# Kernel tuning notes

Hardware: AMD Instinct MI355X
Metric: run time of the kernel (lower is better)

## Reference

```python
import jax, jax.numpy as jnp
import numpy as np

N, E, H, R = 16384, 262144, 256, 64
INV_SQRT_3 = 1.0 / np.sqrt(3.0)
INV_SQRT_H = 1.0 / np.sqrt(float(H))
INV_SQRT_2 = 1.0 / np.sqrt(2.0)


def ssilu(t):
    # ScaledSiLU: silu(x) / 0.6
    return jax.nn.silu(t) * (1.0 / 0.6)


def layernorm(x, g, b):
    m = jnp.mean(x, axis=-1, keepdims=True)
    v = jnp.var(x, axis=-1, keepdims=True)
    return (x - m) * jax.lax.rsqrt(v + 1e-5) * g + b


def gated_equivariant_block(x, v, Wv1, Wv2, Wu1, bu1, Wu2, bu2, out_ch):
    # x: [N, Cin], v: [N, 3, Cin]
    vec1 = jnp.linalg.norm(v @ Wv1, axis=-2)          # [N, Cin]
    vec2 = v @ Wv2                                     # [N, 3, out_ch]
    h = ssilu(jnp.concatenate([x, vec1], axis=-1) @ Wu1 + bu1) @ Wu2 + bu2
    xn, vn = h[..., :out_ch], h[..., out_ch:]
    return ssilu(xn), vn[:, None, :] * vec2


def setup_inputs() -> dict:
    key = jax.random.key(0)
    ks = iter(jax.random.split(key, 48))

    def w(shape, fan_in):
        return jax.random.normal(next(ks), shape, jnp.float32) / np.sqrt(float(fan_in))

    return {
        "x": jax.random.normal(next(ks), (N, H), jnp.float32),
        "vec": jax.random.normal(next(ks), (N, 3, H), jnp.float32),
        "edge_rbf": jax.random.uniform(next(ks), (E, R), jnp.float32),
        "edge_vector": jax.random.normal(next(ks), (E, 3), jnp.float32),
        # PaiNNMessage params
        "ln_g": jnp.ones((H,), jnp.float32), "ln_b": jnp.zeros((H,), jnp.float32),
        "W_x1": w((H, H), H), "b_x1": jnp.zeros((H,), jnp.float32),
        "W_x2": w((H, 3 * H), H), "b_x2": jnp.zeros((3 * H,), jnp.float32),
        "W_rbf": w((R, 3 * H), R), "b_rbf": jnp.zeros((3 * H,), jnp.float32),
        # PaiNNUpdate params
        "W_vp": w((H, 2 * H), H),
        "W_xv1": w((2 * H, H), 2 * H), "b_xv1": jnp.zeros((H,), jnp.float32),
        "W_xv2": w((H, 3 * H), H), "b_xv2": jnp.zeros((3 * H,), jnp.float32),
        # PaiNNOutput block 1 (H -> H//2)
        "o1_Wv1": w((H, H), H), "o1_Wv2": w((H, H // 2), H),
        "o1_Wu1": w((2 * H, H), 2 * H), "o1_bu1": jnp.zeros((H,), jnp.float32),
        "o1_Wu2": w((H, H), H), "o1_bu2": jnp.zeros((H,), jnp.float32),
        # PaiNNOutput block 2 (H//2 -> 1)
        "o2_Wv1": w((H // 2, H // 2), H // 2), "o2_Wv2": w((H // 2, 1), H // 2),
        "o2_Wu1": w((H, H // 2), H), "o2_bu1": jnp.zeros((H // 2,), jnp.float32),
        "o2_Wu2": w((H // 2, 2), H // 2), "o2_bu2": jnp.zeros((2,), jnp.float32),
        "edge_index": jax.random.randint(next(ks), (2, E), 0, N),
    }


def reference(x, vec, edge_rbf, edge_vector,
              ln_g, ln_b, W_x1, b_x1, W_x2, b_x2, W_rbf, b_rbf,
              W_vp, W_xv1, b_xv1, W_xv2, b_xv2,
              o1_Wv1, o1_Wv2, o1_Wu1, o1_bu1, o1_Wu2, o1_bu2,
              o2_Wv1, o2_Wv2, o2_Wu1, o2_bu1, o2_Wu2, o2_bu2,
              edge_index):
    src, dst = edge_index[0], edge_index[1]

    # ---- PaiNNMessage ----
    xh = ssilu(layernorm(x, ln_g, ln_b) @ W_x1 + b_x1) @ W_x2 + b_x2   # [N, 3H]
    rbfh = edge_rbf @ W_rbf + b_rbf                                     # [E, 3H]
    m = xh[src] * rbfh                                                  # gather + fuse
    m1, m2, m3 = m[:, :H], m[:, H:2 * H], m[:, 2 * H:]
    m2 = m2 * INV_SQRT_3
    vmsg = (vec[src] * m2[:, None, :] + m3[:, None, :] * edge_vector[:, :, None]) * INV_SQRT_H  # [E,3,H]
    dx = jax.ops.segment_sum(m1, dst, num_segments=N)
    dvec = jax.ops.segment_sum(vmsg, dst, num_segments=N)
    x = x + dx
    vec = vec + dvec

    # ---- PaiNNUpdate ----
    vp = vec @ W_vp                                    # [N, 3, 2H]
    vec1, vec2 = vp[..., :H], vp[..., H:]
    vec_dot = jnp.sum(vec1 * vec2, axis=1) * INV_SQRT_H            # [N, H]
    vnorm = jnp.sqrt(jnp.sum(vec2 * vec2, axis=-2) + 1e-8)          # [N, H]
    xvh = ssilu(jnp.concatenate([x, vnorm], axis=-1) @ W_xv1 + b_xv1) @ W_xv2 + b_xv2
    xv1, xv2, xv3 = xvh[:, :H], xvh[:, H:2 * H], xvh[:, 2 * H:]
    x = x + (xv1 + xv2 * vec_dot) * INV_SQRT_2
    vec = vec + xv3[:, None, :] * vec1

    # ---- PaiNNOutput ----
    x, vec = gated_equivariant_block(x, vec, o1_Wv1, o1_Wv2, o1_Wu1, o1_bu1, o1_Wu2, o1_bu2, H // 2)
    x, vec = gated_equivariant_block(x, vec, o2_Wv1, o2_Wv2, o2_Wu1, o2_bu1, o2_Wu2, o2_bu2, 1)
    return jnp.squeeze(vec, axis=-1)   # [N, 3]
```

## Files before the change

### kernel.cpp

```cpp
#include <hip/hip_runtime.h>
#include <math.h>

#define NN 16384
#define EE 262144
#define HH 256

#define INV_SQRT_3f 0.57735026918962576f
#define INV_SQRT_Hf 0.0625f
#define INV_SQRT_2f 0.70710678118654752f
#define SSILU_SCALE 1.6666666666666667f

typedef __attribute__((ext_vector_type(8))) short bf16x8;
typedef __attribute__((ext_vector_type(4))) float f32x4;

__device__ __forceinline__ float ssilu_f(float v) {
    return v * (1.0f / (1.0f + __expf(-v))) * SSILU_SCALE;
}
__device__ __forceinline__ float b2f(short s) {
    unsigned int u = ((unsigned int)(unsigned short)s) << 16;
    return __uint_as_float(u);
}
__device__ __forceinline__ short f2b(float f) {
    unsigned int u = __float_as_uint(f);
    unsigned int r = (u + 0x7fff + ((u >> 16) & 1)) >> 16;
    return (short)r;
}

__global__ void __launch_bounds__(256) ln_kernel(const float* __restrict__ x,
                                                 const float* __restrict__ g,
                                                 const float* __restrict__ b,
                                                 short* __restrict__ oh,
                                                 short* __restrict__ ol,
                                                 float* __restrict__ x1) {
    int n = blockIdx.x;
    int t = threadIdx.x;
    float v = x[(long)n * HH + t];
    x1[(long)n * HH + t] = v;
    float s = v, s2 = v * v;
    #pragma unroll
    for (int off = 32; off > 0; off >>= 1) {
        s  += __shfl_down(s, off);
        s2 += __shfl_down(s2, off);
    }
    __shared__ float red[8];
    int wave = t >> 6, lane = t & 63;
    if (lane == 0) { red[wave] = s; red[4 + wave] = s2; }
    __syncthreads();
    __shared__ float mr[2];
    if (t == 0) {
        float ts = red[0] + red[1] + red[2] + red[3];
        float ts2 = red[4] + red[5] + red[6] + red[7];
        float mean = ts * (1.0f / HH);
        float var = ts2 * (1.0f / HH) - mean * mean;
        mr[0] = mean;
        mr[1] = rsqrtf(var + 1e-5f);
    }
    __syncthreads();
    float o = (v - mr[0]) * mr[1] * g[t] + b[t];
    short hh = f2b(o);
    oh[(long)n * HH + t] = hh;
    ol[(long)n * HH + t] = f2b(o - b2f(hh));
}

struct WtArgs {
    const float* W[12];
    int K[12];
    int N[12];
    int off[13];
};

__global__ void __launch_bounds__(256) wt_split_all(WtArgs a,
                                                    short* __restrict__ WTh,
                                                    short* __restrict__ WTl) {
    int idx = blockIdx.x * 256 + threadIdx.x;
    int s = 0;
    #pragma unroll
    for (int i = 1; i < 12; i++) s += (idx >= a.off[i]) ? 1 : 0;
    int local = idx - a.off[s];
    int K = a.K[s], N = a.N[s];
    int k = local / N, n = local - k * N;
    float w = a.W[s][local];
    short hh = f2b(w);
    long o = (long)a.off[s] + (long)n * K + k;
    WTh[o] = hh;
    WTl[o] = f2b(w - b2f(hh));
}

__global__ void __launch_bounds__(256) split4_kernel(const float* __restrict__ in,
                                                     short* __restrict__ h,
                                                     short* __restrict__ l) {
    long i = ((long)blockIdx.x * 256 + threadIdx.x) * 4;
    float4 v = *(const float4*)(in + i);
    short4 oh, ol;
    oh.x = f2b(v.x); ol.x = f2b(v.x - b2f(oh.x));
    oh.y = f2b(v.y); ol.y = f2b(v.y - b2f(oh.y));
    oh.z = f2b(v.z); ol.z = f2b(v.z - b2f(oh.z));
    oh.w = f2b(v.w); ol.w = f2b(v.w - b2f(oh.w));
    *(short4*)(h + i) = oh;
    *(short4*)(l + i) = ol;
}

__global__ void __launch_bounds__(256) mfma_gemm(const short* __restrict__ Ah,
                                                 const short* __restrict__ Al,
                                                 const short* __restrict__ Wh,
                                                 const short* __restrict__ Wl,
                                                 const float* __restrict__ bias,
                                                 void* __restrict__ Ch,
                                                 short* __restrict__ Cl,
                                                 int M, int K, int N, int act) {
    int tid = threadIdx.x;
    int wave = tid >> 6, lane = tid & 63;
    int quad = lane >> 4, l16 = lane & 15;
    long bm = (long)blockIdx.x * 128 + wave * 32;
    long bn = (long)blockIdx.y * 64;
    long a0 = (bm + l16) * K + quad * 8;
    long a1 = a0 + (long)16 * K;
    long w0 = (bn + l16) * K + quad * 8;

    f32x4 acc[2][4];
    #pragma unroll
    for (int f = 0; f < 2; f++)
        #pragma unroll
        for (int t = 0; t < 4; t++) acc[f][t] = (f32x4){0.f, 0.f, 0.f, 0.f};

    bf16x8 cah[2], cal[2], cbh[4], cbl[4];
    cah[0] = *(const bf16x8*)(Ah + a0);
    cah[1] = *(const bf16x8*)(Ah + a1);
    cal[0] = *(const bf16x8*)(Al + a0);
    cal[1] = *(const bf16x8*)(Al + a1);
    #pragma unroll
    for (int t = 0; t < 4; t++) {
        long wo = w0 + (long)t * 16 * K;
        cbh[t] = *(const bf16x8*)(Wh + wo);
        cbl[t] = *(const bf16x8*)(Wl + wo);
    }

    for (int k0 = 0; k0 < K; k0 += 32) {
        int k1 = k0 + 32;
        bf16x8 nah[2], nal[2], nbh[4], nbl[4];
        if (k1 < K) {
            nah[0] = *(const bf16x8*)(Ah + a0 + k1);
            nah[1] = *(const bf16x8*)(Ah + a1 + k1);
            nal[0] = *(const bf16x8*)(Al + a0 + k1);
            nal[1] = *(const bf16x8*)(Al + a1 + k1);
            #pragma unroll
            for (int t = 0; t < 4; t++) {
                long wo = w0 + (long)t * 16 * K + k1;
                nbh[t] = *(const bf16x8*)(Wh + wo);
                nbl[t] = *(const bf16x8*)(Wl + wo);
            }
        }
        #pragma unroll
        for (int t = 0; t < 4; t++) {
            #pragma unroll
            for (int f = 0; f < 2; f++) {
                acc[f][t] = __builtin_amdgcn_mfma_f32_16x16x32_bf16(cah[f], cbh[t], acc[f][t], 0, 0, 0);
                acc[f][t] = __builtin_amdgcn_mfma_f32_16x16x32_bf16(cal[f], cbh[t], acc[f][t], 0, 0, 0);
                acc[f][t] = __builtin_amdgcn_mfma_f32_16x16x32_bf16(cah[f], cbl[t], acc[f][t], 0, 0, 0);
            }
        }
        if (k1 < K) {
            cah[0] = nah[0]; cah[1] = nah[1];
            cal[0] = nal[0]; cal[1] = nal[1];
            #pragma unroll
            for (int t = 0; t < 4; t++) { cbh[t] = nbh[t]; cbl[t] = nbl[t]; }
        }
    }

    #pragma unroll
    for (int f = 0; f < 2; f++) {
        long row0 = bm + f * 16 + quad * 4;
        #pragma unroll
        for (int t = 0; t < 4; t++) {
            long col = bn + t * 16 + l16;
            float bv = bias ? bias[col] : 0.f;
            #pragma unroll
            for (int r = 0; r < 4; r++) {
                float v = acc[f][t][r] + bv;
                if (act & 1) v = ssilu_f(v);
                long idx = (row0 + r) * N + col;
                if (Cl) {
                    short hh = f2b(v);
                    ((short*)Ch)[idx] = hh;
                    Cl[idx] = f2b(v - b2f(hh));
                } else if (act & 2) {
                    ((short*)Ch)[idx] = f2b(v);
                } else {
                    ((float*)Ch)[idx] = v;
                }
            }
        }
    }
}

__global__ void __launch_bounds__(256) zero_kernel(int* __restrict__ p, int n) {
    int i = blockIdx.x * 256 + threadIdx.x;
    if (i < n) p[i] = 0;
}

__global__ void __launch_bounds__(256) hist_kernel(const int* __restrict__ eidx,
                                                   int* __restrict__ cnt) {
    int e = blockIdx.x * 256 + threadIdx.x;
    atomicAdd(&cnt[eidx[EE + e]], 1);
}

__global__ void __launch_bounds__(256) scan_kernel(int* __restrict__ cursor,
                                                   int* __restrict__ rowptr) {
    int t = threadIdx.x;
    int base_i = t * 64;
    int tsum = 0;
    for (int i = 0; i < 64; i++) tsum += cursor[base_i + i];
    __shared__ int ls[256];
    ls[t] = tsum;
    __syncthreads();
    for (int off = 1; off < 256; off <<= 1) {
        int v = (t >= off) ? ls[t - off] : 0;
        __syncthreads();
        ls[t] += v;
        __syncthreads();
    }
    int running = ls[t] - tsum;
    for (int i = 0; i < 64; i++) {
        int c = cursor[base_i + i];
        rowptr[base_i + i] = running;
        cursor[base_i + i] = running;
        running += c;
    }
    if (t == 255) rowptr[NN] = running;
}

__global__ void __launch_bounds__(256) scatter_kernel(const int* __restrict__ eidx,
                                                      const float* __restrict__ ev,
                                                      int* __restrict__ cursor,
                                                      int* __restrict__ perm,
                                                      int* __restrict__ dsts,
                                                      int* __restrict__ srcs,
                                                      float* __restrict__ evs) {
    int e = blockIdx.x * 256 + threadIdx.x;
    int s_ = eidx[e];
    int d_ = eidx[EE + e];
    int pos = atomicAdd(&cursor[d_], 1);
    perm[pos] = e;
    dsts[pos] = d_;
    srcs[pos] = s_;
    evs[pos * 3 + 0] = ev[e * 3 + 0];
    evs[pos * 3 + 1] = ev[e * 3 + 1];
    evs[pos * 3 + 2] = ev[e * 3 + 2];
}

__global__ void __launch_bounds__(512) edge_gather_kernel(
        const float* __restrict__ rbf,
        const short* __restrict__ Wrh,
        const short* __restrict__ Wrl,
        const float* __restrict__ b_rbf,
        const float* __restrict__ xh,
        const float* __restrict__ vec,
        const int* __restrict__ perm,
        const int* __restrict__ dsts,
        const int* __restrict__ srcs,
        const float* __restrict__ evs,
        float* __restrict__ x1,
        float* __restrict__ vecacc) {
    int tid = threadIdx.x;
    int wave = tid >> 6, lane = tid & 63;
    int quad = lane >> 4, l16 = lane & 15;
    int bm = blockIdx.x * 128;
    int base = wave * 16;

    __shared__ __align__(16) float mlds[128][66];
    __shared__ int dst_s[128], src_s[128];
    __shared__ float ev_s[128][3];

    if (lane < 16) {
        int i = base + lane;
        dst_s[i] = dsts[bm + i];
        src_s[i] = srcs[bm + i];
        ev_s[i][0] = evs[(long)(bm + i) * 3 + 0];
        ev_s[i][1] = evs[(long)(bm + i) * 3 + 1];
        ev_s[i][2] = evs[(long)(bm + i) * 3 + 2];
    }

    int e0 = perm[bm + base + l16];
    bf16x8 afh[2], afl[2];
    {
        long ebase = (long)e0 * 64 + quad * 8;
        #pragma unroll
        for (int ks = 0; ks < 2; ks++) {
            float4 ua = *(const float4*)(rbf + ebase + ks * 32);
            float4 ub = *(const float4*)(rbf + ebase + ks * 32 + 4);
            float vv[8] = {ua.x, ua.y, ua.z, ua.w, ub.x, ub.y, ub.z, ub.w};
            bf16x8 hh, ll;
            #pragma unroll
            for (int j = 0; j < 8; j++) {
                short hb = f2b(vv[j]);
                hh[j] = hb;
                ll[j] = f2b(vv[j] - b2f(hb));
            }
            afh[ks] = hh;
            afl[ks] = ll;
        }
    }

    for (int sec = 0; sec < 3; sec++) {
        for (int tile = 0; tile < 4; tile++) {
            int bn = sec * 256 + tile * 64;
            f32x4 acc[4];
            #pragma unroll
            for (int t = 0; t < 4; t++) {
                float bv = b_rbf[bn + t * 16 + l16];
                acc[t] = (f32x4){bv, bv, bv, bv};
                #pragma unroll
                for (int ks = 0; ks < 2; ks++) {
                    long wo = (long)(bn + t * 16 + l16) * 64 + ks * 32 + quad * 8;
                    bf16x8 bh = *(const bf16x8*)(Wrh + wo);
                    bf16x8 bl = *(const bf16x8*)(Wrl + wo);
                    acc[t] = __builtin_amdgcn_mfma_f32_16x16x32_bf16(afh[ks], bh, acc[t], 0, 0, 0);
                    acc[t] = __builtin_amdgcn_mfma_f32_16x16x32_bf16(afl[ks], bh, acc[t], 0, 0, 0);
                    acc[t] = __builtin_amdgcn_mfma_f32_16x16x32_bf16(afh[ks], bl, acc[t], 0, 0, 0);
                }
            }
            #pragma unroll
            for (int t = 0; t < 4; t++)
                #pragma unroll
                for (int r = 0; r < 4; r++)
                    mlds[base + quad * 4 + r][t * 16 + l16] = acc[t][r];

            int colx = tile * 64 + lane;
            if (sec == 0) {
                float pv[16];
                #pragma unroll
                for (int i = 0; i < 16; i++) {
                    long xb = (long)src_s[base + i] * 768;
                    pv[i] = mlds[base + i][lane] * xh[xb + colx];
                }
                float a = 0.f;
                int dprev = dst_s[base];
                #pragma unroll
                for (int i = 0; i < 16; i++) {
                    int d = dst_s[base + i];
                    if (d != dprev) {
                        atomicAdd(&x1[(long)dprev * 256 + colx], a);
                        a = 0.f;
                        dprev = d;
                    }
                    a += pv[i];
                }
                atomicAdd(&x1[(long)dprev * 256 + colx], a);
            } else if (sec == 1) {
                float a0 = 0.f, a1 = 0.f, a2 = 0.f;
                int dprev = dst_s[base];
                #pragma unroll 1
                for (int b = 0; b < 4; b++) {
                    float p0[4], p1[4], p2[4];
                    #pragma unroll
                    for (int j = 0; j < 4; j++) {
                        int i = b * 4 + j;
                        long xb = (long)src_s[base + i] * 768;
                        float m2 = mlds[base + i][lane] * (INV_SQRT_3f * INV_SQRT_Hf) *
                                   xh[xb + 256 + colx];
                        p0[j] = vec[xb + colx] * m2;
                        p1[j] = vec[xb + 256 + colx] * m2;
                        p2[j] = vec[xb + 512 + colx] * m2;
                    }
                    #pragma unroll
                    for (int j = 0; j < 4; j++) {
                        int i = b * 4 + j;
                        int d = dst_s[base + i];
                        if (d != dprev) {
                            long vb = (long)dprev * 768 + colx;
                            atomicAdd(&vecacc[vb], a0);
                            atomicAdd(&vecacc[vb + 256], a1);
                            atomicAdd(&vecacc[vb + 512], a2);
                            a0 = a1 = a2 = 0.f;
                            dprev = d;
                        }
                        a0 += p0[j]; a1 += p1[j]; a2 += p2[j];
                    }
                }
                long vb = (long)dprev * 768 + colx;
                atomicAdd(&vecacc[vb], a0);
                atomicAdd(&vecacc[vb + 256], a1);
                atomicAdd(&vecacc[vb + 512], a2);
            } else {
                float pm[16];
                #pragma unroll
                for (int i = 0; i < 16; i++) {
                    long xb = (long)src_s[base + i] * 768;
                    pm[i] = mlds[base + i][lane] * INV_SQRT_Hf * xh[xb + 512 + colx];
                }
                float a0 = 0.f, a1 = 0.f, a2 = 0.f;
                int dprev = dst_s[base];
                #pragma unroll
                for (int i = 0; i < 16; i++) {
                    int d = dst_s[base + i];
                    if (d != dprev) {
                        long vb = (long)dprev * 768 + colx;
                        atomicAdd(&vecacc[vb], a0);
                        atomicAdd(&vecacc[vb + 256], a1);
                        atomicAdd(&vecacc[vb + 512], a2);
                        a0 = a1 = a2 = 0.f;
                        dprev = d;
                    }
                    a0 += pm[i] * ev_s[base + i][0];
                    a1 += pm[i] * ev_s[base + i][1];
                    a2 += pm[i] * ev_s[base + i][2];
                }
                long vb = (long)dprev * 768 + colx;
                atomicAdd(&vecacc[vb], a0);
                atomicAdd(&vecacc[vb + 256], a1);
                atomicAdd(&vecacc[vb + 512], a2);
            }
        }
    }
}

__global__ void __launch_bounds__(256) vdot_cat_kernel(const float* __restrict__ vec1,
                                                       const short* __restrict__ vec2,
                                                       const float* __restrict__ x1,
                                                       float* __restrict__ vdot,
                                                       short* __restrict__ cath,
                                                       short* __restrict__ catl) {
    int idx = blockIdx.x * 256 + threadIdx.x;
    int n = idx >> 8, h = idx & 255;
    float dsum = 0.f, s2 = 0.f;
    #pragma unroll
    for (int d = 0; d < 3; d++) {
        long r = (long)(n * 3 + d) * 256 + h;
        float a = vec1[r];
        float b = b2f(vec2[r]);
        dsum += a * b;
        s2 += b * b;
    }
    vdot[idx] = dsum * INV_SQRT_Hf;
    float xv = x1[idx];
    short hh = f2b(xv);
    cath[(long)n * 512 + h] = hh;
    catl[(long)n * 512 + h] = f2b(xv - b2f(hh));
    float vn = sqrtf(s2 + 1e-8f);
    short vh = f2b(vn);
    cath[(long)n * 512 + 256 + h] = vh;
    catl[(long)n * 512 + 256 + h] = f2b(vn - b2f(vh));
}

__global__ void __launch_bounds__(256) e4_kernel(float* __restrict__ x1,
                                                 float* __restrict__ vecacc,
                                                 const float* __restrict__ vec1,
                                                 const float* __restrict__ vdot,
                                                 const short* __restrict__ xvh_h,
                                                 const short* __restrict__ xvh_l) {
    int idx = blockIdx.x * 256 + threadIdx.x;
    int n = idx >> 8, h = idx & 255;
    long b0 = (long)n * 768 + h;
    float xv1 = b2f(xvh_h[b0])       + b2f(xvh_l[b0]);
    float xv2 = b2f(xvh_h[b0 + 256]) + b2f(xvh_l[b0 + 256]);
    float xv3 = b2f(xvh_h[b0 + 512]) + b2f(xvh_l[b0 + 512]);
    x1[idx] = x1[idx] + (xv1 + xv2 * vdot[idx]) * INV_SQRT_2f;
    #pragma unroll
    for (int d = 0; d < 3; d++) {
        long r = (long)(n * 3 + d) * 256 + h;
        vecacc[r] = vecacc[r] + xv3 * vec1[r];
    }
}

__global__ void __launch_bounds__(256) normcat_kernel(const float* __restrict__ xin,
                                                      const short* __restrict__ w,
                                                      short* __restrict__ cath,
                                                      short* __restrict__ catl,
                                                      int Cx, int C, int shift) {
    int idx = blockIdx.x * 256 + threadIdx.x;
    int cols = 1 << shift;
    int n = idx >> shift, c = idx & (cols - 1);
    float v;
    if (c < Cx) {
        v = xin[(long)n * Cx + c];
    } else {
        int cc = c - Cx;
        float s = 0.f;
        #pragma unroll
        for (int d = 0; d < 3; d++) {
            float a = b2f(w[(long)(n * 3 + d) * C + cc]);
            s += a * a;
        }
        v = sqrtf(s);
    }
    short hh = f2b(v);
    cath[idx] = hh;
    catl[idx] = f2b(v - b2f(hh));
}

__global__ void __launch_bounds__(256) gate1_kernel(const float* __restrict__ h1,
                                                    const short* __restrict__ w2h,
                                                    const short* __restrict__ w2l,
                                                    float* __restrict__ x3,
                                                    short* __restrict__ vecCh,
                                                    short* __restrict__ vecCl) {
    int idx = blockIdx.x * 256 + threadIdx.x;
    int n = idx >> 7, c = idx & 127;
    x3[idx] = ssilu_f(h1[(long)n * 256 + c]);
    float vn = h1[(long)n * 256 + 128 + c];
    #pragma unroll
    for (int d = 0; d < 3; d++) {
        long r = (long)(n * 3 + d) * 128 + c;
        float wv = b2f(w2h[r]) + b2f(w2l[r]);
        float v = vn * wv;
        short hh = f2b(v);
        vecCh[r] = hh;
        vecCl[r] = f2b(v - b2f(hh));
    }
}

__global__ void __launch_bounds__(256) g12_kernel(const short* __restrict__ vecCh,
                                                  const short* __restrict__ vecCl,
                                                  const float* __restrict__ Wv2,
                                                  float* __restrict__ w4) {
    int row = blockIdx.x * 4 + (threadIdx.x >> 6);
    int lane = threadIdx.x & 63;
    long r0 = (long)row * 128 + lane;
    float v0 = b2f(vecCh[r0]) + b2f(vecCl[r0]);
    float v1 = b2f(vecCh[r0 + 64]) + b2f(vecCl[r0 + 64]);
    float s = v0 * Wv2[lane] + v1 * Wv2[64 + lane];
    #pragma unroll
    for (int off = 32; off > 0; off >>= 1) s += __shfl_down(s, off);
    if (lane == 0) w4[row] = s;
}

__global__ void __launch_bounds__(256) final_kernel(const float* __restrict__ t5,
                                                    const float* __restrict__ Wu2,
                                                    const float* __restrict__ bu2,
                                                    const float* __restrict__ w4,
                                                    float* __restrict__ out) {
    int n = blockIdx.x * 4 + (threadIdx.x >> 6);
    int lane = threadIdx.x & 63;
    float s = t5[(long)n * 128 + lane] * Wu2[lane * 2 + 1] +
              t5[(long)n * 128 + 64 + lane] * Wu2[(64 + lane) * 2 + 1];
    #pragma unroll
    for (int off = 32; off > 0; off >>= 1) s += __shfl_down(s, off);
    float val = __shfl(s, 0) + bu2[1];
    if (lane < 3) out[(long)n * 3 + lane] = val * w4[(long)n * 3 + lane];
}

extern "C" void kernel_launch(void* const* d_in, const int* in_sizes, int n_in,
                              void* d_out, int out_size, void* d_ws, size_t ws_size,
                              hipStream_t stream) {
    const float* x          = (const float*)d_in[0];
    const float* vec        = (const float*)d_in[1];
    const float* edge_rbf   = (const float*)d_in[2];
    const float* edge_vector= (const float*)d_in[3];
    const float* ln_g       = (const float*)d_in[4];
    const float* ln_b       = (const float*)d_in[5];
    const float* W_x1       = (const float*)d_in[6];
    const float* b_x1       = (const float*)d_in[7];
    const float* W_x2       = (const float*)d_in[8];
    const float* b_x2       = (const float*)d_in[9];
    const float* W_rbf      = (const float*)d_in[10];
    const float* b_rbf      = (const float*)d_in[11];
    const float* W_vp       = (const float*)d_in[12];
    const float* W_xv1      = (const float*)d_in[13];
    const float* b_xv1      = (const float*)d_in[14];
    const float* W_xv2      = (const float*)d_in[15];
    const float* b_xv2      = (const float*)d_in[16];
    const float* o1_Wv1     = (const float*)d_in[17];
    const float* o1_Wv2     = (const float*)d_in[18];
    const float* o1_Wu1     = (const float*)d_in[19];
    const float* o1_bu1     = (const float*)d_in[20];
    const float* o1_Wu2     = (const float*)d_in[21];
    const float* o1_bu2     = (const float*)d_in[22];
    const float* o2_Wv1     = (const float*)d_in[23];
    const float* o2_Wv2     = (const float*)d_in[24];
    const float* o2_Wu1     = (const float*)d_in[25];
    const float* o2_bu1     = (const float*)d_in[26];
    const float* o2_Wu2     = (const float*)d_in[27];
    const float* o2_bu2     = (const float*)d_in[28];
    const int*   edge_index = (const int*)d_in[29];
    float* out = (float*)d_out;
    float* ws  = (float*)d_ws;

    const size_t S = (size_t)NN * 256;
    const size_t Q = S / 4;
    float* x1      = ws;
    float* vecacc  = ws + 4 * Q;
    short* wtb     = (short*)(ws + 16 * Q);
    const long WLO = 1114112;
    short* xln_h = (short*)(ws + 18 * Q);
    short* xln_l = (short*)(ws + 20 * Q);
    short* t1_h  = (short*)(ws + 22 * Q);
    short* t1_l  = (short*)(ws + 24 * Q);
    float* xh    = ws + 30 * Q;
    int* rowptr    = (int*)(ws + 48 * Q);
    int* cursor    = rowptr + (NN + 1);
    int* perm      = cursor + NN;
    int* dsts      = perm + EE;
    int* srcs      = dsts + EE;
    float* evs     = (float*)(srcs + EE);
    short* vah   = (short*)(ws + 18 * Q);
    short* val_  = (short*)(ws + 24 * Q);
    float* vec1  = ws + 30 * Q;
    short* vec2b = (short*)(ws + 42 * Q);
    float* vdot  = ws + 48 * Q;
    short* catb_h = (short*)(ws + 18 * Q);
    short* catb_l = (short*)(ws + 22 * Q);
    short* t2_h  = (short*)(ws + 26 * Q);
    short* t2_l  = (short*)(ws + 28 * Q);
    short* xvh_h = (short*)(ws + 18 * Q);
    short* xvh_l = (short*)(ws + 42 * Q);
    short* vah2  = (short*)(ws + 18 * Q);
    short* val2  = (short*)(ws + 24 * Q);
    short* w1b   = (short*)(ws + 30 * Q);
    short* w2_h  = (short*)(ws + 36 * Q);
    short* w2_l  = (short*)(ws + 39 * Q);
    short* cat2_h = (short*)(ws + 42 * Q);
    short* cat2_l = (short*)(ws + 46 * Q);
    short* t4_h  = (short*)(ws + 18 * Q);
    short* t4_l  = (short*)(ws + 20 * Q);
    float* h1    = ws + 22 * Q;
    float* x3    = ws + 26 * Q;
    short* vecC_h = (short*)(ws + 28 * Q);
    short* vecC_l = (short*)(ws + 31 * Q);
    short* w3b   = (short*)(ws + 34 * Q);
    float* w4    = ws + 37 * Q;
    short* cat3_h = (short*)(ws + 38 * Q);
    short* cat3_l = (short*)(ws + 40 * Q);
    float* t5    = ws + 42 * Q;

    short* WT_x1    = wtb;
    short* WT_x2    = wtb + 65536;
    short* WT_vp    = wtb + 262144;
    short* WT_xv1   = wtb + 393216;
    short* WT_xv2   = wtb + 524288;
    short* WT_o1Wv1 = wtb + 720896;
    short* WT_o1Wv2 = wtb + 786432;
    short* WT_o1Wu1 = wtb + 819200;
    short* WT_o1Wu2 = wtb + 950272;
    short* WT_o2Wv1 = wtb + 1015808;
    short* WT_o2Wu1 = wtb + 1032192;
    short* WT_rbf   = wtb + 1064960;

    WtArgs wa;
    const float* wsrc[12] = {W_x1, W_x2, W_vp, W_xv1, W_xv2, o1_Wv1, o1_Wv2,
                             o1_Wu1, o1_Wu2, o2_Wv1, o2_Wu1, W_rbf};
    int wk[12] = {256, 256, 256, 512, 256, 256, 256, 512, 256, 128, 256, 64};
    int wn[12] = {256, 768, 512, 256, 768, 256, 128, 256, 256, 128, 128, 768};
    int off = 0;
    for (int i = 0; i < 12; i++) {
        wa.W[i] = wsrc[i]; wa.K[i] = wk[i]; wa.N[i] = wn[i];
        wa.off[i] = off; off += wk[i] * wn[i];
    }
    wa.off[12] = off;
    wt_split_all<<<off / 256, 256, 0, stream>>>(wa, wtb, wtb + WLO);

    hipMemcpyAsync(vecacc, vec, 3 * S * sizeof(float), hipMemcpyDeviceToDevice, stream);

    ln_kernel<<<NN, 256, 0, stream>>>(x, ln_g, ln_b, xln_h, xln_l, x1);
    mfma_gemm<<<dim3(NN / 128, 4), 256, 0, stream>>>(xln_h, xln_l, WT_x1, WT_x1 + WLO,
                                                     b_x1, t1_h, t1_l, NN, 256, 256, 1);
    mfma_gemm<<<dim3(NN / 128, 12), 256, 0, stream>>>(t1_h, t1_l, WT_x2, WT_x2 + WLO,
                                                      b_x2, xh, nullptr, NN, 256, 768, 0);

    zero_kernel<<<(NN + 255) / 256, 256, 0, stream>>>(cursor, NN);
    hist_kernel<<<EE / 256, 256, 0, stream>>>(edge_index, cursor);
    scan_kernel<<<1, 256, 0, stream>>>(cursor, rowptr);
    scatter_kernel<<<EE / 256, 256, 0, stream>>>(edge_index, edge_vector, cursor,
                                                 perm, dsts, srcs, evs);
    edge_gather_kernel<<<EE / 128, 512, 0, stream>>>(
        edge_rbf, WT_rbf, WT_rbf + WLO, b_rbf, xh, vec,
        perm, dsts, srcs, evs, x1, vecacc);
    split4_kernel<<<3 * S / 1024, 256, 0, stream>>>(vecacc, vah, val_);

    mfma_gemm<<<dim3(3 * NN / 128, 4), 256, 0, stream>>>(vah, val_, WT_vp, WT_vp + WLO,
                                                         nullptr, vec1, nullptr,
                                                         3 * NN, 256, 256, 0);
    mfma_gemm<<<dim3(3 * NN / 128, 4), 256, 0, stream>>>(vah, val_, WT_vp + 65536,
                                                         WT_vp + WLO + 65536,
                                                         nullptr, vec2b, nullptr,
                                                         3 * NN, 256, 256, 2);
    vdot_cat_kernel<<<NN, 256, 0, stream>>>(vec1, vec2b, x1, vdot, catb_h, catb_l);
    mfma_gemm<<<dim3(NN / 128, 4), 256, 0, stream>>>(catb_h, catb_l, WT_xv1, WT_xv1 + WLO,
                                                     b_xv1, t2_h, t2_l, NN, 512, 256, 1);
    mfma_gemm<<<dim3(NN / 128, 12), 256, 0, stream>>>(t2_h, t2_l, WT_xv2, WT_xv2 + WLO,
                                                      b_xv2, xvh_h, xvh_l, NN, 256, 768, 0);
    e4_kernel<<<NN, 256, 0, stream>>>(x1, vecacc, vec1, vdot, xvh_h, xvh_l);

    split4_kernel<<<3 * S / 1024, 256, 0, stream>>>(vecacc, vah2, val2);
    mfma_gemm<<<dim3(3 * NN / 128, 4), 256, 0, stream>>>(vah2, val2, WT_o1Wv1, WT_o1Wv1 + WLO,
                                                         nullptr, w1b, nullptr,
                                                         3 * NN, 256, 256, 2);
    mfma_gemm<<<dim3(3 * NN / 128, 2), 256, 0, stream>>>(vah2, val2, WT_o1Wv2, WT_o1Wv2 + WLO,
                                                         nullptr, w2_h, w2_l,
                                                         3 * NN, 256, 128, 0);
    normcat_kernel<<<NN * 512 / 256, 256, 0, stream>>>(x1, w1b, cat2_h, cat2_l, 256, 256, 9);
    mfma_gemm<<<dim3(NN / 128, 4), 256, 0, stream>>>(cat2_h, cat2_l, WT_o1Wu1, WT_o1Wu1 + WLO,
                                                     o1_bu1, t4_h, t4_l, NN, 512, 256, 1);
    mfma_gemm<<<dim3(NN / 128, 4), 256, 0, stream>>>(t4_h, t4_l, WT_o1Wu2, WT_o1Wu2 + WLO,
                                                     o1_bu2, h1, nullptr, NN, 256, 256, 0);
    gate1_kernel<<<NN * 128 / 256, 256, 0, stream>>>(h1, w2_h, w2_l, x3, vecC_h, vecC_l);

    mfma_gemm<<<dim3(3 * NN / 128, 2), 256, 0, stream>>>(vecC_h, vecC_l, WT_o2Wv1,
                                                         WT_o2Wv1 + WLO, nullptr,
                                                         w3b, nullptr, 3 * NN, 128, 128, 2);
    g12_kernel<<<3 * NN / 4, 256, 0, stream>>>(vecC_h, vecC_l, o2_Wv2, w4);
    normcat_kernel<<<NN * 256 / 256, 256, 0, stream>>>(x3, w3b, cat3_h, cat3_l, 128, 128, 8);
    mfma_gemm<<<dim3(NN / 128, 2), 256, 0, stream>>>(cat3_h, cat3_l, WT_o2Wu1, WT_o2Wu1 + WLO,
                                                     o2_bu1, t5, nullptr, NN, 256, 128, 1);
    final_kernel<<<NN / 4, 256, 0, stream>>>(t5, o2_Wu2, o2_bu2, w4, out);
}
```

Before: 1.459 ms.

## Convert fp32 activations to bf16 hi/lo inside GEMM and merge sibling GEMMs

The GEMM now reads fp32 activations and splits them into bf16 hi/lo pairs in registers, so the split4 kernels and the hi/lo outputs of the producer kernels go away. The two W_vp GEMMs and the two o1 Wv GEMMs, which share the same input, are each merged into one launch with a wider N and a split epilogue. This cuts kernel launches and intermediate traffic. In exchange, the A loads double in bytes per element and the conversion ALU work is repeated in every N-tile block.

```diff
diff --git a/kernel.cpp b/kernel.cpp
--- a/kernel.cpp
+++ b/kernel.cpp
@@ -25,12 +25,20 @@
     unsigned int r = (u + 0x7fff + ((u >> 16) & 1)) >> 16;
     return (short)r;
 }
+__device__ __forceinline__ void cvt8(float4 a, float4 b, bf16x8& h, bf16x8& l) {
+    float v[8] = {a.x, a.y, a.z, a.w, b.x, b.y, b.z, b.w};
+    #pragma unroll
+    for (int j = 0; j < 8; j++) {
+        short hh = f2b(v[j]);
+        h[j] = hh;
+        l[j] = f2b(v[j] - b2f(hh));
+    }
+}
 
 __global__ void __launch_bounds__(256) ln_kernel(const float* __restrict__ x,
                                                  const float* __restrict__ g,
                                                  const float* __restrict__ b,
-                                                 short* __restrict__ oh,
-                                                 short* __restrict__ ol,
+                                                 float* __restrict__ o_,
                                                  float* __restrict__ x1) {
     int n = blockIdx.x;
     int t = threadIdx.x;
@@ -56,10 +64,7 @@
         mr[1] = rsqrtf(var + 1e-5f);
     }
     __syncthreads();
-    float o = (v - mr[0]) * mr[1] * g[t] + b[t];
-    short hh = f2b(o);
-    oh[(long)n * HH + t] = hh;
-    ol[(long)n * HH + t] = f2b(o - b2f(hh));
+    o_[(long)n * HH + t] = (v - mr[0]) * mr[1] * g[t] + b[t];
 }
 
 struct WtArgs {
@@ -86,27 +91,12 @@
     WTl[o] = f2b(w - b2f(hh));
 }
 
-__global__ void __launch_bounds__(256) split4_kernel(const float* __restrict__ in,
-                                                     short* __restrict__ h,
-                                                     short* __restrict__ l) {
-    long i = ((long)blockIdx.x * 256 + threadIdx.x) * 4;
-    float4 v = *(const float4*)(in + i);
-    short4 oh, ol;
-    oh.x = f2b(v.x); ol.x = f2b(v.x - b2f(oh.x));
-    oh.y = f2b(v.y); ol.y = f2b(v.y - b2f(oh.y));
-    oh.z = f2b(v.z); ol.z = f2b(v.z - b2f(oh.z));
-    oh.w = f2b(v.w); ol.w = f2b(v.w - b2f(oh.w));
-    *(short4*)(h + i) = oh;
-    *(short4*)(l + i) = ol;
-}
-
-__global__ void __launch_bounds__(256) mfma_gemm(const short* __restrict__ Ah,
-                                                 const short* __restrict__ Al,
+__global__ void __launch_bounds__(256) mfma_gemm(const float* __restrict__ A,
                                                  const short* __restrict__ Wh,
                                                  const short* __restrict__ Wl,
                                                  const float* __restrict__ bias,
-                                                 void* __restrict__ Ch,
-                                                 short* __restrict__ Cl,
+                                                 void* __restrict__ C1,
+                                                 void* __restrict__ C2,
                                                  int M, int K, int N, int act) {
     int tid = threadIdx.x;
     int wave = tid >> 6, lane = tid & 63;
@@ -124,10 +114,8 @@
         for (int t = 0; t < 4; t++) acc[f][t] = (f32x4){0.f, 0.f, 0.f, 0.f};
 
     bf16x8 cah[2], cal[2], cbh[4], cbl[4];
-    cah[0] = *(const bf16x8*)(Ah + a0);
-    cah[1] = *(const bf16x8*)(Ah + a1);
-    cal[0] = *(const bf16x8*)(Al + a0);
-    cal[1] = *(const bf16x8*)(Al + a1);
+    cvt8(*(const float4*)(A + a0), *(const float4*)(A + a0 + 4), cah[0], cal[0]);
+    cvt8(*(const float4*)(A + a1), *(const float4*)(A + a1 + 4), cah[1], cal[1]);
     #pragma unroll
     for (int t = 0; t < 4; t++) {
         long wo = w0 + (long)t * 16 * K;
@@ -137,12 +125,13 @@
 
     for (int k0 = 0; k0 < K; k0 += 32) {
         int k1 = k0 + 32;
-        bf16x8 nah[2], nal[2], nbh[4], nbl[4];
+        float4 n0a, n0b, n1a, n1b;
+        bf16x8 nbh[4], nbl[4];
         if (k1 < K) {
-            nah[0] = *(const bf16x8*)(Ah + a0 + k1);
-            nah[1] = *(const bf16x8*)(Ah + a1 + k1);
-            nal[0] = *(const bf16x8*)(Al + a0 + k1);
-            nal[1] = *(const bf16x8*)(Al + a1 + k1);
+            n0a = *(const float4*)(A + a0 + k1);
+            n0b = *(const float4*)(A + a0 + k1 + 4);
+            n1a = *(const float4*)(A + a1 + k1);
+            n1b = *(const float4*)(A + a1 + k1 + 4);
             #pragma unroll
             for (int t = 0; t < 4; t++) {
                 long wo = w0 + (long)t * 16 * K + k1;
@@ -160,8 +149,8 @@
             }
         }
         if (k1 < K) {
-            cah[0] = nah[0]; cah[1] = nah[1];
-            cal[0] = nal[0]; cal[1] = nal[1];
+            cvt8(n0a, n0b, cah[0], cal[0]);
+            cvt8(n1a, n1b, cah[1], cal[1]);
             #pragma unroll
             for (int t = 0; t < 4; t++) { cbh[t] = nbh[t]; cbl[t] = nbl[t]; }
         }
@@ -177,16 +166,25 @@
             #pragma unroll
             for (int r = 0; r < 4; r++) {
                 float v = acc[f][t][r] + bv;
-                if (act & 1) v = ssilu_f(v);
-                long idx = (row0 + r) * N + col;
-                if (Cl) {
-                    short hh = f2b(v);
-                    ((short*)Ch)[idx] = hh;
-                    Cl[idx] = f2b(v - b2f(hh));
-                } else if (act & 2) {
-                    ((short*)Ch)[idx] = f2b(v);
+                long row = row0 + r;
+                if (act == 4) {
+                    if (col < 256) ((float*)C1)[row * 256 + col] = v;
+                    else           ((short*)C2)[row * 256 + col - 256] = f2b(v);
+                } else if (act == 5) {
+                    if (col < 256) ((short*)C1)[row * 256 + col] = f2b(v);
+                    else           ((float*)C2)[row * 128 + col - 256] = v;
                 } else {
-                    ((float*)Ch)[idx] = v;
+                    long idx = row * N + col;
+                    if (act == 3) {
+                        short hh = f2b(v);
+                        ((short*)C1)[idx] = hh;
+                        ((short*)C2)[idx] = f2b(v - b2f(hh));
+                    } else if (act == 2) {
+                        ((short*)C1)[idx] = f2b(v);
+                    } else {
+                        if (act == 1) v = ssilu_f(v);
+                        ((float*)C1)[idx] = v;
+                    }
                 }
             }
         }
@@ -288,16 +286,7 @@
         for (int ks = 0; ks < 2; ks++) {
             float4 ua = *(const float4*)(rbf + ebase + ks * 32);
             float4 ub = *(const float4*)(rbf + ebase + ks * 32 + 4);
-            float vv[8] = {ua.x, ua.y, ua.z, ua.w, ub.x, ub.y, ub.z, ub.w};
-            bf16x8 hh, ll;
-            #pragma unroll
-            for (int j = 0; j < 8; j++) {
-                short hb = f2b(vv[j]);
-                hh[j] = hb;
-                ll[j] = f2b(vv[j] - b2f(hb));
-            }
-            afh[ks] = hh;
-            afl[ks] = ll;
+            cvt8(ua, ub, afh[ks], afl[ks]);
         }
     }
 
@@ -418,8 +407,7 @@
                                                        const short* __restrict__ vec2,
                                                        const float* __restrict__ x1,
                                                        float* __restrict__ vdot,
-                                                       short* __restrict__ cath,
-                                                       short* __restrict__ catl) {
+                                                       float* __restrict__ cat) {
     int idx = blockIdx.x * 256 + threadIdx.x;
     int n = idx >> 8, h = idx & 255;
     float dsum = 0.f, s2 = 0.f;
@@ -432,14 +420,8 @@
         s2 += b * b;
     }
     vdot[idx] = dsum * INV_SQRT_Hf;
-    float xv = x1[idx];
-    short hh = f2b(xv);
-    cath[(long)n * 512 + h] = hh;
-    catl[(long)n * 512 + h] = f2b(xv - b2f(hh));
-    float vn = sqrtf(s2 + 1e-8f);
-    short vh = f2b(vn);
-    cath[(long)n * 512 + 256 + h] = vh;
-    catl[(long)n * 512 + 256 + h] = f2b(vn - b2f(vh));
+    cat[(long)n * 512 + h] = x1[idx];
+    cat[(long)n * 512 + 256 + h] = sqrtf(s2 + 1e-8f);
 }
 
 __global__ void __launch_bounds__(256) e4_kernel(float* __restrict__ x1,
@@ -464,8 +446,7 @@
 
 __global__ void __launch_bounds__(256) normcat_kernel(const float* __restrict__ xin,
                                                       const short* __restrict__ w,
-                                                      short* __restrict__ cath,
-                                                      short* __restrict__ catl,
+                                                      float* __restrict__ cat,
                                                       int Cx, int C, int shift) {
     int idx = blockIdx.x * 256 + threadIdx.x;
     int cols = 1 << shift;
@@ -483,17 +464,13 @@
         }
         v = sqrtf(s);
     }
-    short hh = f2b(v);
-    cath[idx] = hh;
-    catl[idx] = f2b(v - b2f(hh));
+    cat[idx] = v;
 }
 
 __global__ void __launch_bounds__(256) gate1_kernel(const float* __restrict__ h1,
-                                                    const short* __restrict__ w2h,
-                                                    const short* __restrict__ w2l,
+                                                    const float* __restrict__ w2,
                                                     float* __restrict__ x3,
-                                                    short* __restrict__ vecCh,
-                                                    short* __restrict__ vecCl) {
+                                                    float* __restrict__ vecC) {
     int idx = blockIdx.x * 256 + threadIdx.x;
     int n = idx >> 7, c = idx & 127;
     x3[idx] = ssilu_f(h1[(long)n * 256 + c]);
@@ -501,24 +478,17 @@
     #pragma unroll
     for (int d = 0; d < 3; d++) {
         long r = (long)(n * 3 + d) * 128 + c;
-        float wv = b2f(w2h[r]) + b2f(w2l[r]);
-        float v = vn * wv;
-        short hh = f2b(v);
-        vecCh[r] = hh;
-        vecCl[r] = f2b(v - b2f(hh));
-    }
-}
-
-__global__ void __launch_bounds__(256) g12_kernel(const short* __restrict__ vecCh,
-                                                  const short* __restrict__ vecCl,
+        vecC[r] = vn * w2[r];
+    }
+}
+
+__global__ void __launch_bounds__(256) g12_kernel(const float* __restrict__ vecC,
                                                   const float* __restrict__ Wv2,
                                                   float* __restrict__ w4) {
     int row = blockIdx.x * 4 + (threadIdx.x >> 6);
     int lane = threadIdx.x & 63;
     long r0 = (long)row * 128 + lane;
-    float v0 = b2f(vecCh[r0]) + b2f(vecCl[r0]);
-    float v1 = b2f(vecCh[r0 + 64]) + b2f(vecCl[r0 + 64]);
-    float s = v0 * Wv2[lane] + v1 * Wv2[64 + lane];
+    float s = vecC[r0] * Wv2[lane] + vecC[r0 + 64] * Wv2[64 + lane];
     #pragma unroll
     for (int off = 32; off > 0; off >>= 1) s += __shfl_down(s, off);
     if (lane == 0) w4[row] = s;
@@ -581,10 +551,8 @@
     float* vecacc  = ws + 4 * Q;
     short* wtb     = (short*)(ws + 16 * Q);
     const long WLO = 1114112;
-    short* xln_h = (short*)(ws + 18 * Q);
-    short* xln_l = (short*)(ws + 20 * Q);
-    short* t1_h  = (short*)(ws + 22 * Q);
-    short* t1_l  = (short*)(ws + 24 * Q);
+    float* xln   = ws + 18 * Q;
+    float* t1    = ws + 22 * Q;
     float* xh    = ws + 30 * Q;
     int* rowptr    = (int*)(ws + 48 * Q);
     int* cursor    = rowptr + (NN + 1);
@@ -592,34 +560,23 @@
     int* dsts      = perm + EE;
     int* srcs      = dsts + EE;
     float* evs     = (float*)(srcs + EE);
-    short* vah   = (short*)(ws + 18 * Q);
-    short* val_  = (short*)(ws + 24 * Q);
     float* vec1  = ws + 30 * Q;
     short* vec2b = (short*)(ws + 42 * Q);
     float* vdot  = ws + 48 * Q;
-    short* catb_h = (short*)(ws + 18 * Q);
-    short* catb_l = (short*)(ws + 22 * Q);
-    short* t2_h  = (short*)(ws + 26 * Q);
-    short* t2_l  = (short*)(ws + 28 * Q);
+    float* cat   = ws + 18 * Q;
+    float* t2    = ws + 26 * Q;
     short* xvh_h = (short*)(ws + 18 * Q);
     short* xvh_l = (short*)(ws + 42 * Q);
-    short* vah2  = (short*)(ws + 18 * Q);
-    short* val2  = (short*)(ws + 24 * Q);
     short* w1b   = (short*)(ws + 30 * Q);
-    short* w2_h  = (short*)(ws + 36 * Q);
-    short* w2_l  = (short*)(ws + 39 * Q);
-    short* cat2_h = (short*)(ws + 42 * Q);
-    short* cat2_l = (short*)(ws + 46 * Q);
-    short* t4_h  = (short*)(ws + 18 * Q);
-    short* t4_l  = (short*)(ws + 20 * Q);
+    float* w2    = ws + 36 * Q;
+    float* cat2  = ws + 42 * Q;
+    float* t4    = ws + 18 * Q;
     float* h1    = ws + 22 * Q;
     float* x3    = ws + 26 * Q;
-    short* vecC_h = (short*)(ws + 28 * Q);
-    short* vecC_l = (short*)(ws + 31 * Q);
+    float* vecC  = ws + 28 * Q;
     short* w3b   = (short*)(ws + 34 * Q);
     float* w4    = ws + 37 * Q;
-    short* cat3_h = (short*)(ws + 38 * Q);
-    short* cat3_l = (short*)(ws + 40 * Q);
+    float* cat3  = ws + 38 * Q;
     float* t5    = ws + 42 * Q;
 
     short* WT_x1    = wtb;
@@ -650,10 +607,10 @@
 
     hipMemcpyAsync(vecacc, vec, 3 * S * sizeof(float), hipMemcpyDeviceToDevice, stream);
 
-    ln_kernel<<<NN, 256, 0, stream>>>(x, ln_g, ln_b, xln_h, xln_l, x1);
-    mfma_gemm<<<dim3(NN / 128, 4), 256, 0, stream>>>(xln_h, xln_l, WT_x1, WT_x1 + WLO,
-                                                     b_x1, t1_h, t1_l, NN, 256, 256, 1);
-    mfma_gemm<<<dim3(NN / 128, 12), 256, 0, stream>>>(t1_h, t1_l, WT_x2, WT_x2 + WLO,
+    ln_kernel<<<NN, 256, 0, stream>>>(x, ln_g, ln_b, xln, x1);
+    mfma_gemm<<<dim3(NN / 128, 4), 256, 0, stream>>>(xln, WT_x1, WT_x1 + WLO,
+                                                     b_x1, t1, nullptr, NN, 256, 256, 1);
+    mfma_gemm<<<dim3(NN / 128, 12), 256, 0, stream>>>(t1, WT_x2, WT_x2 + WLO,
                                                       b_x2, xh, nullptr, NN, 256, 768, 0);
 
     zero_kernel<<<(NN + 255) / 256, 256, 0, stream>>>(cursor, NN);
@@ -664,42 +621,33 @@
     edge_gather_kernel<<<EE / 128, 512, 0, stream>>>(
         edge_rbf, WT_rbf, WT_rbf + WLO, b_rbf, xh, vec,
         perm, dsts, srcs, evs, x1, vecacc);
-    split4_kernel<<<3 * S / 1024, 256, 0, stream>>>(vecacc, vah, val_);
-
-    mfma_gemm<<<dim3(3 * NN / 128, 4), 256, 0, stream>>>(vah, val_, WT_vp, WT_vp + WLO,
-                                                         nullptr, vec1, nullptr,
-                                                         3 * NN, 256, 256, 0);
-    mfma_gemm<<<dim3(3 * NN / 128, 4), 256, 0, stream>>>(vah, val_, WT_vp + 65536,
-                                                         WT_vp + WLO + 65536,
-                                                         nullptr, vec2b, nullptr,
-                                                         3 * NN, 256, 256, 2);
-    vdot_cat_kernel<<<NN, 256, 0, stream>>>(vec1, vec2b, x1, vdot, catb_h, catb_l);
-    mfma_gemm<<<dim3(NN / 128, 4), 256, 0, stream>>>(catb_h, catb_l, WT_xv1, WT_xv1 + WLO,
-                                                     b_xv1, t2_h, t2_l, NN, 512, 256, 1);
-    mfma_gemm<<<dim3(NN / 128, 12), 256, 0, stream>>>(t2_h, t2_l, WT_xv2, WT_xv2 + WLO,
-                                                      b_xv2, xvh_h, xvh_l, NN, 256, 768, 0);
+
+    mfma_gemm<<<dim3(3 * NN / 128, 8), 256, 0, stream>>>(vecacc, WT_vp, WT_vp + WLO,
+                                                         nullptr, vec1, vec2b,
+                                                         3 * NN, 256, 512, 4);
+    vdot_cat_kernel<<<NN, 256, 0, stream>>>(vec1, vec2b, x1, vdot, cat);
+    mfma_gemm<<<dim3(NN / 128, 4), 256, 0, stream>>>(cat, WT_xv1, WT_xv1 + WLO,
+                                                     b_xv1, t2, nullptr, NN, 512, 256, 1);
+    mfma_gemm<<<dim3(NN / 128, 12), 256, 0, stream>>>(t2, WT_xv2, WT_xv2 + WLO,
+                                                      b_xv2, xvh_h, xvh_l, NN, 256, 768, 3);
     e4_kernel<<<NN, 256, 0, stream>>>(x1, vecacc, vec1, vdot, xvh_h, xvh_l);
 
-    split4_kernel<<<3 * S / 1024, 256, 0, stream>>>(vecacc, vah2, val2);
-    mfma_gemm<<<dim3(3 * NN / 128, 4), 256, 0, stream>>>(vah2, val2, WT_o1Wv1, WT_o1Wv1 + WLO,
-                                                         nullptr, w1b, nullptr,
-                                                         3 * NN, 256, 256, 2);
-    mfma_gemm<<<dim3(3 * NN / 128, 2), 256, 0, stream>>>(vah2, val2, WT_o1Wv2, WT_o1Wv2 + WLO,
-                                                         nullptr, w2_h, w2_l,
-                                                         3 * NN, 256, 128, 0);
-    normcat_kernel<<<NN * 512 / 256, 256, 0, stream>>>(x1, w1b, cat2_h, cat2_l, 256, 256, 9);
-    mfma_gemm<<<dim3(NN / 128, 4), 256, 0, stream>>>(cat2_h, cat2_l, WT_o1Wu1, WT_o1Wu1 + WLO,
-                                                     o1_bu1, t4_h, t4_l, NN, 512, 256, 1);
-    mfma_gemm<<<dim3(NN / 128, 4), 256, 0, stream>>>(t4_h, t4_l, WT_o1Wu2, WT_o1Wu2 + WLO,
+    mfma_gemm<<<dim3(3 * NN / 128, 6), 256, 0, stream>>>(vecacc, WT_o1Wv1, WT_o1Wv1 + WLO,
+                                                         nullptr, w1b, w2,
+                                                         3 * NN, 256, 384, 5);
+    normcat_kernel<<<NN * 512 / 256, 256, 0, stream>>>(x1, w1b, cat2, 256, 256, 9);
+    mfma_gemm<<<dim3(NN / 128, 4), 256, 0, stream>>>(cat2, WT_o1Wu1, WT_o1Wu1 + WLO,
+                                                     o1_bu1, t4, nullptr, NN, 512, 256, 1);
+    mfma_gemm<<<dim3(NN / 128, 4), 256, 0, stream>>>(t4, WT_o1Wu2, WT_o1Wu2 + WLO,
                                                      o1_bu2, h1, nullptr, NN, 256, 256, 0);
-    gate1_kernel<<<NN * 128 / 256, 256, 0, stream>>>(h1, w2_h, w2_l, x3, vecC_h, vecC_l);
-
-    mfma_gemm<<<dim3(3 * NN / 128, 2), 256, 0, stream>>>(vecC_h, vecC_l, WT_o2Wv1,
-                                                         WT_o2Wv1 + WLO, nullptr,
-                                                         w3b, nullptr, 3 * NN, 128, 128, 2);
-    g12_kernel<<<3 * NN / 4, 256, 0, stream>>>(vecC_h, vecC_l, o2_Wv2, w4);
-    normcat_kernel<<<NN * 256 / 256, 256, 0, stream>>>(x3, w3b, cat3_h, cat3_l, 128, 128, 8);
-    mfma_gemm<<<dim3(NN / 128, 2), 256, 0, stream>>>(cat3_h, cat3_l, WT_o2Wu1, WT_o2Wu1 + WLO,
+    gate1_kernel<<<NN * 128 / 256, 256, 0, stream>>>(h1, w2, x3, vecC);
+
+    mfma_gemm<<<dim3(3 * NN / 128, 2), 256, 0, stream>>>(vecC, WT_o2Wv1, WT_o2Wv1 + WLO,
+                                                         nullptr, w3b, nullptr,
+                                                         3 * NN, 128, 128, 2);
+    g12_kernel<<<3 * NN / 4, 256, 0, stream>>>(vecC, o2_Wv2, w4);
+    normcat_kernel<<<NN * 256 / 256, 256, 0, stream>>>(x3, w3b, cat3, 128, 128, 8);
+    mfma_gemm<<<dim3(NN / 128, 2), 256, 0, stream>>>(cat3, WT_o2Wu1, WT_o2Wu1 + WLO,
                                                      o2_bu1, t5, nullptr, NN, 256, 128, 1);
     final_kernel<<<NN / 4, 256, 0, stream>>>(t5, o2_Wu2, o2_bu2, w4, out);
 }
```

Measured after the change: 1.455 ms. About the same (-0.3%).
